# Kernel tuning notes

Measured on AMD Instinct MI355X. Metric: run time of the kernel, lower is better.

Reference implementation:

```python
import jax, jax.numpy as jnp
import numpy as np
import math

# Model dims (see shape_source)
N_EMBD = 2048
QK_H = 128      # per-head qk dim
V_H = 128       # per-head v dim
Q_DIM = N_EMBD                 # 2048 -> 16 query heads
N_HEAD = Q_DIM // QK_H         # 16
KV_HEAD = N_HEAD // 4          # 4 (GQA)
K_DIM = KV_HEAD * QK_H         # 512
V_DIM = KV_HEAD * V_H          # 512
D_KV = K_DIM + V_DIM           # 1024, S6 channel dim
D_STATE = 16                   # S6 state size
DT_RANK = math.ceil(D_KV / 16) # 'auto' -> 64
WINDOW = 512
B, T = 1, 4096


def setup_inputs() -> dict:
    key = jax.random.key(0)
    ks = jax.random.split(key, 8)
    x = jax.random.normal(ks[0], (B, T, N_EMBD), jnp.float32)
    W_attn = jax.random.normal(ks[1], (Q_DIM + K_DIM + V_DIM, N_EMBD), jnp.float32) * 0.02
    # S6 params (canonical Mamba S6 init: A = -exp(A_log), A_log = log(1..N))
    A_log = jnp.log(jnp.arange(1, D_STATE + 1, dtype=jnp.float32))[None, :] * jnp.ones((D_KV, 1), jnp.float32)
    x_proj_w = jax.random.normal(ks[2], (DT_RANK + 2 * D_STATE, D_KV), jnp.float32) * 0.02
    dt_proj_w = jax.random.normal(ks[3], (D_KV, DT_RANK), jnp.float32) * 0.02
    dt_proj_b = jax.random.normal(ks[4], (D_KV,), jnp.float32) * 0.1
    D_param = jnp.ones((D_KV,), jnp.float32)
    W_o = jax.random.normal(ks[5], (N_EMBD, Q_DIM), jnp.float32) * 0.02
    return dict(x=x, W_attn=W_attn, A_log=A_log, x_proj_w=x_proj_w,
                dt_proj_w=dt_proj_w, dt_proj_b=dt_proj_b, D_param=D_param,
                W_o=W_o, window_size=WINDOW)


def s6_scan(u, A_log, x_proj_w, dt_proj_w, dt_proj_b, D_param):
    """Canonical S6 selective scan. u: (B, T, D) -> (B, T, D)."""
    Bb, Tt, D = u.shape
    N = A_log.shape[1]
    dt_rank = dt_proj_w.shape[1]
    x_dbl = jnp.einsum('btd,ed->bte', u, x_proj_w)          # (B,T,dt_rank+2N)
    dt, Bm, Cm = jnp.split(x_dbl, [dt_rank, dt_rank + N], axis=-1)
    delta = jax.nn.softplus(jnp.einsum('btr,dr->btd', dt, dt_proj_w) + dt_proj_b)  # (B,T,D)
    A = -jnp.exp(A_log)                                      # (D,N), negative
    dA = jnp.exp(delta[..., None] * A)                       # (B,T,D,N)
    dBu = delta[..., None] * Bm[:, :, None, :] * u[..., None]  # (B,T,D,N)

    def step(h, inp):
        dA_t, dBu_t, C_t = inp
        h = dA_t * h + dBu_t                                 # (B,D,N)
        y = jnp.einsum('bdn,bn->bd', h, C_t)
        return h, y

    h0 = jnp.zeros((Bb, D, N), u.dtype)
    _, ys = jax.lax.scan(step, h0,
                         (dA.transpose(1, 0, 2, 3), dBu.transpose(1, 0, 2, 3), Cm.transpose(1, 0, 2)))
    y = ys.transpose(1, 0, 2)                                # (B,T,D)
    return y + D_param * u


def sliding_window_attn(q, k, v, window, scale):
    """Causal sliding-window attention; query i attends to j in [i-(window-1), i].
    q: (B,T,H,dh), k/v: (B,T,Hk,dh). Blockwise with one look-back block."""
    Bb, Tt, H, dh = q.shape
    Hk = k.shape[2]
    G = H // Hk
    k = jnp.repeat(k, G, axis=2)
    v = jnp.repeat(v, G, axis=2)
    W = window
    nb = Tt // W
    # (B,H,nb,W,dh)
    qb = q.reshape(Bb, nb, W, H, dh).transpose(0, 3, 1, 2, 4)
    kb = k.reshape(Bb, nb, W, H, dh).transpose(0, 3, 1, 2, 4)
    vb = v.reshape(Bb, nb, W, H, dh).transpose(0, 3, 1, 2, 4)
    # previous block (zeros for first block)
    kprev = jnp.pad(kb, ((0, 0), (0, 0), (1, 0), (0, 0), (0, 0)))[:, :, :nb]
    vprev = jnp.pad(vb, ((0, 0), (0, 0), (1, 0), (0, 0), (0, 0)))[:, :, :nb]
    k2 = jnp.concatenate([kprev, kb], axis=3)                # (B,H,nb,2W,dh)
    v2 = jnp.concatenate([vprev, vb], axis=3)
    scores = jnp.einsum('bhwid,bhwjd->bhwij', qb * scale, k2)  # (B,H,nb,W,2W)
    i = jnp.arange(W)[:, None]
    j = jnp.arange(2 * W)[None, :]
    rel = i + W - j                                          # absolute i - j
    base_mask = (rel >= 0) & (rel <= W - 1)                  # causal & within window
    blk = jnp.arange(nb)[:, None, None]
    valid = base_mask[None] & ((j[None] >= W) | (blk > 0))   # first block: no look-back
    neg = jnp.finfo(jnp.float32).max
    scores = jnp.where(valid[None, None], scores, -neg)
    attn = jax.nn.softmax(scores.astype(jnp.float32), axis=-1).astype(q.dtype)
    out = jnp.einsum('bhwij,bhwjd->bhwid', attn, v2)         # (B,H,nb,W,dh)
    return out.transpose(0, 2, 3, 1, 4).reshape(Bb, Tt, H, dh)


def reference(x, W_attn, A_log, x_proj_w, dt_proj_w, dt_proj_b, D_param, W_o, window_size):
    Bb, Tt, C = x.shape
    qkv = jnp.einsum('btc,oc->bto', x, W_attn)
    q = qkv[..., :Q_DIM]
    kv = qkv[..., Q_DIM:]
    kv = s6_scan(kv, A_log, x_proj_w, dt_proj_w, dt_proj_b, D_param)
    k = kv[..., :K_DIM]
    v = kv[..., K_DIM:]
    q = q.reshape(Bb, Tt, N_HEAD, QK_H)
    k = k.reshape(Bb, Tt, KV_HEAD, QK_H)
    v = v.reshape(Bb, Tt, KV_HEAD, V_H)
    scale = 1.0 / math.sqrt(QK_H)
    y = sliding_window_attn(q, k, v, window_size, scale)     # (B,T,H,v_h)
    y = y.reshape(Bb, Tt, -1)
    return jnp.einsum('bto,no->btn', y, W_o)
```

## Files before the change

### kernel.cpp

```cpp
#include <hip/hip_runtime.h>
#include <hip/hip_bf16.h>

typedef __hip_bfloat16 bf16;
typedef __attribute__((ext_vector_type(8))) short bf16x8;
typedef __attribute__((ext_vector_type(4))) float f32x4;

#define T_SEQ 4096
#define NEMBD 2048
#define QKVD  3072
#define QDIM  2048
#define DKV   1024
#define KDIM  512
#define NH    16
#define DH    128
#define NST   16
#define DTR   64
#define WIN   512
#define NCHUNK 128
#define CLEN   32

__device__ inline float bf2f(bf16 x) { return __bfloat162float(x); }

struct F8 { float v[8]; };

__device__ inline F8 load_b8(const bf16* p) {
  union { uint4 q; unsigned short s[8]; } u;
  u.q = *reinterpret_cast<const uint4*>(p);
  F8 r;
#pragma unroll
  for (int i = 0; i < 8; i++) r.v[i] = __uint_as_float((unsigned)u.s[i] << 16);
  return r;
}

__device__ inline F8 load8(const void* base, size_t idx, int f32flag) {
  if (f32flag) {
    const float4* p = reinterpret_cast<const float4*>((const float*)base + idx);
    float4 a = p[0], b = p[1];
    F8 r;
    r.v[0]=a.x; r.v[1]=a.y; r.v[2]=a.z; r.v[3]=a.w;
    r.v[4]=b.x; r.v[5]=b.y; r.v[6]=b.z; r.v[7]=b.w;
    return r;
  }
  return load_b8((const bf16*)base + idx);
}

__device__ inline float load1(const void* base, size_t idx, int f32flag) {
  return f32flag ? ((const float*)base)[idx] : bf2f(((const bf16*)base)[idx]);
}

__device__ inline unsigned short f2b_bits(float f) {
  bf16 h = __float2bfloat16(f);
  union { bf16 h; unsigned short u; } c; c.h = h; return c.u;
}

__device__ inline ushort4 pack4(float a, float b, float c, float d) {
  ushort4 r; r.x = f2b_bits(a); r.y = f2b_bits(b); r.z = f2b_bits(c); r.w = f2b_bits(d);
  return r;
}

__device__ inline void gld_lds16(const void* g, void* l) {
  __builtin_amdgcn_global_load_lds(
      (const __attribute__((address_space(1))) unsigned int*)g,
      (__attribute__((address_space(3))) unsigned int*)l, 16, 0, 0);
}

__global__ void detect_dtype(const unsigned short* __restrict__ x, int* __restrict__ flag) {
  if (threadIdx.x == 0 && blockIdx.x == 0) {
    int c = 0;
    for (int i = 0; i < 128; i++) {
      float v = __uint_as_float((unsigned)x[i] << 16);
      float a = fabsf(v);
      if (a >= 1e-8f && a <= 1e4f) c++;
    }
    flag[0] = (c >= 120) ? 0 : 1;
  }
}

__global__ __launch_bounds__(256) void cvt_bf16(
    const void* __restrict__ in, const int* __restrict__ dflag,
    unsigned short* __restrict__ out, int n8)
{
  int i = blockIdx.x * 256 + threadIdx.x;
  if (i >= n8) return;
  const int f = dflag[0];
  F8 v = load8(in, (size_t)i * 8, f);
  ushort4* o = (ushort4*)(out + (size_t)i * 8);
  o[0] = pack4(v.v[0], v.v[1], v.v[2], v.v[3]);
  o[1] = pack4(v.v[4], v.v[5], v.v[6], v.v[7]);
}

__global__ __launch_bounds__(512, 2) void gemm_wide(
    const unsigned short* __restrict__ A, const unsigned short* __restrict__ B,
    int M, int N, int K, int mode,
    bf16* __restrict__ oq, bf16* __restrict__ ou, float* __restrict__ oc)
{
  __shared__ unsigned short lds[2][384 * 64];
  const int tid = threadIdx.x;
  const int wave = tid >> 6, lane = tid & 63;
  const int quad = lane >> 4, l16 = lane & 15;
  const int wm = wave >> 1, wn = wave & 1;
  const int nbx = N >> 7;
  const int nwg = gridDim.x;
  const int chunk = nwg >> 3;
  const int swz = (blockIdx.x & 7) * chunk + (blockIdx.x >> 3);
  const int bm = (swz / nbx) * 256, bn = (swz % nbx) * 128;

  const int lrow = lane >> 3;
  const int lslot = (lane & 7) ^ lrow;
  const unsigned short* Abase = A + (size_t)(bm + wave * 8 + lrow) * K + lslot * 8;
  const unsigned short* Bbase = B + (size_t)(bn + wave * 8 + lrow) * K + lslot * 8;

  const int x7 = l16 & 7;
  const int s0 = ((0 + quad) ^ x7) * 8;
  const int s1 = ((4 + quad) ^ x7) * 8;
  const int arow0 = (wm * 64 + l16) * 64;
  const int brow0 = (256 + wn * 64 + l16) * 64;

  f32x4 acc[4][4];
#pragma unroll
  for (int i = 0; i < 4; i++)
#pragma unroll
    for (int j = 0; j < 4; j++) acc[i][j] = f32x4{0.f, 0.f, 0.f, 0.f};

  const int NT = K >> 6;

#pragma unroll
  for (int grp = 0; grp < 4; grp++)
    gld_lds16(Abase + (size_t)grp * 64 * K, &lds[0][(grp * 64 + wave * 8) * 64]);
#pragma unroll
  for (int grp = 0; grp < 2; grp++)
    gld_lds16(Bbase + (size_t)grp * 64 * K, &lds[0][(256 + grp * 64 + wave * 8) * 64]);
#pragma unroll
  for (int grp = 0; grp < 4; grp++)
    gld_lds16(Abase + (size_t)grp * 64 * K + 64, &lds[1][(grp * 64 + wave * 8) * 64]);
#pragma unroll
  for (int grp = 0; grp < 2; grp++)
    gld_lds16(Bbase + (size_t)grp * 64 * K + 64, &lds[1][(256 + grp * 64 + wave * 8) * 64]);
  asm volatile("s_waitcnt vmcnt(6)" ::: "memory");
  __builtin_amdgcn_sched_barrier(0);
  __builtin_amdgcn_s_barrier();

#define MM(m, n) \
  acc[m][n] = __builtin_amdgcn_mfma_f32_16x16x32_bf16(aF[m][0], bF[n][0], acc[m][n], 0, 0, 0); \
  acc[m][n] = __builtin_amdgcn_mfma_f32_16x16x32_bf16(aF[m][1], bF[n][1], acc[m][n], 0, 0, 0);

  for (int g = 0; g < NT; ++g) {
    const unsigned short* L = lds[g & 1];
    unsigned short* Lw = (unsigned short*)L;
    const bool stF = (g + 2) < NT;
    const size_t kF = (size_t)(g + 2) * 64;

    bf16x8 aF[4][2], bF[4][2];

#pragma unroll
    for (int m = 0; m < 4; m++) {
      aF[m][0] = *(const bf16x8*)&L[arow0 + m * 1024 + s0];
      aF[m][1] = *(const bf16x8*)&L[arow0 + m * 1024 + s1];
    }
    bF[0][0] = *(const bf16x8*)&L[brow0 +    0 + s0];
    bF[0][1] = *(const bf16x8*)&L[brow0 +    0 + s1];
    bF[1][0] = *(const bf16x8*)&L[brow0 + 1024 + s0];
    bF[1][1] = *(const bf16x8*)&L[brow0 + 1024 + s1];
    __builtin_amdgcn_s_barrier();
    if (stF) {
#pragma unroll
      for (int grp = 0; grp < 4; grp++)
        gld_lds16(Abase + (size_t)grp * 64 * K + kF, &Lw[(grp * 64 + wave * 8) * 64]);
    }
    __builtin_amdgcn_s_setprio(1);
    MM(0,0); MM(0,1); MM(1,0); MM(1,1);
    MM(2,0); MM(2,1); MM(3,0); MM(3,1);
    __builtin_amdgcn_s_setprio(0);
    __builtin_amdgcn_s_barrier();

    bF[2][0] = *(const bf16x8*)&L[brow0 + 2048 + s0];
    bF[2][1] = *(const bf16x8*)&L[brow0 + 2048 + s1];
    bF[3][0] = *(const bf16x8*)&L[brow0 + 3072 + s0];
    bF[3][1] = *(const bf16x8*)&L[brow0 + 3072 + s1];
    __builtin_amdgcn_s_barrier();
    if (stF) {
#pragma unroll
      for (int grp = 0; grp < 2; grp++)
        gld_lds16(Bbase + (size_t)grp * 64 * K + kF, &Lw[(256 + grp * 64 + wave * 8) * 64]);
    }
    __builtin_amdgcn_s_setprio(1);
    MM(0,2); MM(0,3); MM(1,2); MM(1,3);
    MM(2,2); MM(2,3); MM(3,2); MM(3,3);
    __builtin_amdgcn_s_setprio(0);
    if (stF) { asm volatile("s_waitcnt vmcnt(6)" ::: "memory"); }
    else     { asm volatile("s_waitcnt vmcnt(0)" ::: "memory"); }
    __builtin_amdgcn_sched_barrier(0);
    __builtin_amdgcn_s_barrier();
  }
#undef MM

#pragma unroll
  for (int m = 0; m < 4; m++)
#pragma unroll
    for (int n = 0; n < 4; n++) {
      int gm0 = bm + wm * 64 + m * 16 + quad * 4;
      int gn  = bn + wn * 64 + n * 16 + l16;
#pragma unroll
      for (int r = 0; r < 4; r++) {
        int gm = gm0 + r;
        float v = acc[m][n][r];
        if (mode == 0) {
          if (gn < QDIM) oq[(size_t)gm * QDIM + gn] = __float2bfloat16(v);
          else           ou[(size_t)gm * DKV + (gn - QDIM)] = __float2bfloat16(v);
        } else {
          oc[(size_t)gm * N + gn] = v;
        }
      }
    }
}

__global__ __launch_bounds__(256) void xdbl_mfma(
    const bf16* __restrict__ u, const unsigned short* __restrict__ xpw_bf,
    float* __restrict__ xd)
{
  __shared__ unsigned short Us[64 * 32];
  __shared__ unsigned short Ws[96 * 32];
  const int tid = threadIdx.x;
  const int wave = tid >> 6, lane = tid & 63;
  const int quad = lane >> 4, l16 = lane & 15;
  const int t0 = blockIdx.x * 64;
  const unsigned short* ub = (const unsigned short*)u;

  f32x4 acc[6];
#pragma unroll
  for (int j = 0; j < 6; j++) acc[j] = f32x4{0.f, 0.f, 0.f, 0.f};

  const int urow = tid >> 2, ucol = (tid & 3) * 8;
  const int wrow0 = tid >> 2, wcol0 = (tid & 3) * 8;
  const int wrow1 = (256 + tid) >> 2;

  uint4 upre = *(const uint4*)(ub + (size_t)(t0 + urow) * DKV + ucol);
  uint4 wpre0 = *(const uint4*)(xpw_bf + (size_t)wrow0 * DKV + wcol0);
  uint4 wpre1 = (tid < 128) ? *(const uint4*)(xpw_bf + (size_t)wrow1 * DKV + wcol0)
                            : uint4{0, 0, 0, 0};

  for (int k0 = 0; k0 < DKV; k0 += 32) {
    __syncthreads();
    *(uint4*)&Us[urow * 32 + ucol] = upre;
    *(uint4*)&Ws[wrow0 * 32 + wcol0] = wpre0;
    if (tid < 128) *(uint4*)&Ws[wrow1 * 32 + wcol0] = wpre1;
    __syncthreads();

    int kn = (k0 + 32 < DKV) ? (k0 + 32) : k0;
    upre  = *(const uint4*)(ub + (size_t)(t0 + urow) * DKV + kn + ucol);
    wpre0 = *(const uint4*)(xpw_bf + (size_t)wrow0 * DKV + kn + wcol0);
    if (tid < 128) wpre1 = *(const uint4*)(xpw_bf + (size_t)wrow1 * DKV + kn + wcol0);

    bf16x8 a = *(const bf16x8*)&Us[(wave * 16 + l16) * 32 + quad * 8];
#pragma unroll
    for (int j = 0; j < 6; j++) {
      bf16x8 b = *(const bf16x8*)&Ws[(j * 16 + l16) * 32 + quad * 8];
      acc[j] = __builtin_amdgcn_mfma_f32_16x16x32_bf16(a, b, acc[j], 0, 0, 0);
    }
  }

#pragma unroll
  for (int j = 0; j < 6; j++)
#pragma unroll
    for (int r = 0; r < 4; r++) {
      int t = t0 + wave * 16 + quad * 4 + r;
      xd[(size_t)t * 96 + j * 16 + l16] = acc[j][r];
    }
}

__global__ __launch_bounds__(256) void delta_mfma(
    const float* __restrict__ xd, const unsigned short* __restrict__ dtw_bf,
    const void* __restrict__ dtb, const int* __restrict__ dflag,
    bf16* __restrict__ delta)
{
  __shared__ unsigned short Xs[64 * 72];
  __shared__ unsigned short Ws[128 * 72];
  const int tid = threadIdx.x;
  const int wave = tid >> 6, lane = tid & 63;
  const int quad = lane >> 4, l16 = lane & 15;
  const int t0 = blockIdx.y * 64, d0 = blockIdx.x * 128;

  for (int e = tid; e < 64 * 8; e += 256) {
    int row = e >> 3, c8 = (e & 7) * 8;
    const float* p = xd + (size_t)(t0 + row) * 96 + c8;
    float4 a = *(const float4*)p, b = *(const float4*)(p + 4);
    *(ushort4*)&Xs[row * 72 + c8]     = pack4(a.x, a.y, a.z, a.w);
    *(ushort4*)&Xs[row * 72 + c8 + 4] = pack4(b.x, b.y, b.z, b.w);
  }
  for (int e = tid; e < 128 * 8; e += 256) {
    int row = e >> 3, c8 = (e & 7) * 8;
    *(uint4*)&Ws[row * 72 + c8] = *(const uint4*)(dtw_bf + (size_t)(d0 + row) * DTR + c8);
  }
  __syncthreads();

  bf16x8 a0 = *(const bf16x8*)&Xs[(wave * 16 + l16) * 72 + quad * 8];
  bf16x8 a1 = *(const bf16x8*)&Xs[(wave * 16 + l16) * 72 + 32 + quad * 8];

  f32x4 acc[8];
#pragma unroll
  for (int j = 0; j < 8; j++) {
    bf16x8 b0 = *(const bf16x8*)&Ws[(j * 16 + l16) * 72 + quad * 8];
    bf16x8 b1 = *(const bf16x8*)&Ws[(j * 16 + l16) * 72 + 32 + quad * 8];
    acc[j] = __builtin_amdgcn_mfma_f32_16x16x32_bf16(a0, b0, f32x4{0.f, 0.f, 0.f, 0.f}, 0, 0, 0);
    acc[j] = __builtin_amdgcn_mfma_f32_16x16x32_bf16(a1, b1, acc[j], 0, 0, 0);
  }

  const int f = dflag[0];
#pragma unroll
  for (int j = 0; j < 8; j++) {
    int d = d0 + j * 16 + l16;
    float bias = load1(dtb, d, f);
#pragma unroll
    for (int r = 0; r < 4; r++) {
      int t = t0 + wave * 16 + quad * 4 + r;
      float v = acc[j][r] + bias;
      float sp = fmaxf(v, 0.f) + log1pf(expf(-fabsf(v)));
      delta[(size_t)t * DKV + d] = __float2bfloat16(sp);
    }
  }
}

__global__ __launch_bounds__(256) void scan_pass1(
    const bf16* __restrict__ delta, const bf16* __restrict__ u,
    const float* __restrict__ xd, const void* __restrict__ A_log,
    const int* __restrict__ dflag, float* __restrict__ Pb, float* __restrict__ Hl)
{
  const int gid = blockIdx.x * 256 + threadIdx.x;
  const int c = gid >> 14;
  const int r = gid & 16383;
  const int d = r >> 4, n = r & 15;
  const int f = dflag[0];
  const float A = -expf(load1(A_log, d * NST + n, f));
  float p = 1.f, h = 0.f;
  const int t0 = c * CLEN;
  for (int tt = 0; tt < CLEN; tt++) {
    int t = t0 + tt;
    float dl = bf2f(delta[(size_t)t * DKV + d]);
    float uu = bf2f(u[(size_t)t * DKV + d]);
    float bm = xd[(size_t)t * 96 + DTR + n];
    float a = expf(dl * A);
    h = a * h + dl * bm * uu;
    p *= a;
  }
  Pb[gid] = p;
  Hl[gid] = h;
}

__global__ __launch_bounds__(256) void scan_combine(
    float* __restrict__ Pb, const float* __restrict__ Hl)
{
  const int idx = blockIdx.x * 256 + threadIdx.x;
  float run = 0.f;
  for (int c = 0; c < NCHUNK; c++) {
    size_t off = (size_t)c * 16384 + idx;
    float p = Pb[off], hl = Hl[off];
    Pb[off] = run;
    run = p * run + hl;
  }
}

__global__ __launch_bounds__(256) void scan_pass2(
    const bf16* __restrict__ delta, bf16* __restrict__ u,
    const float* __restrict__ xd, const void* __restrict__ A_log,
    const void* __restrict__ Dp, const int* __restrict__ dflag,
    const float* __restrict__ Hin)
{
  const int gid = blockIdx.x * 256 + threadIdx.x;
  const int c = gid >> 14;
  const int r = gid & 16383;
  const int d = r >> 4, n = r & 15;
  const int f = dflag[0];
  const float A = -expf(load1(A_log, d * NST + n, f));
  const float dpar = load1(Dp, d, f);
  float h = Hin[gid];
  const int t0 = c * CLEN;
  for (int tt = 0; tt < CLEN; tt++) {
    int t = t0 + tt;
    float dl = bf2f(delta[(size_t)t * DKV + d]);
    float uu = bf2f(u[(size_t)t * DKV + d]);
    float bm = xd[(size_t)t * 96 + DTR + n];
    float cm = xd[(size_t)t * 96 + DTR + NST + n];
    float a = expf(dl * A);
    h = a * h + dl * bm * uu;
    float part = h * cm;
    part += __shfl_xor(part, 1);
    part += __shfl_xor(part, 2);
    part += __shfl_xor(part, 4);
    part += __shfl_xor(part, 8);
    if (n == 0) u[(size_t)t * DKV + d] = __float2bfloat16(part + dpar * uu);
  }
}

__global__ __launch_bounds__(256) void vtrans(
    const bf16* __restrict__ kv, unsigned short* __restrict__ vt)
{
  __shared__ float tile[64][68];
  const int tt0 = blockIdx.x * 64, d0 = blockIdx.y * 64;
  const int tid = threadIdx.x;
  for (int e = tid; e < 64 * 8; e += 256) {
    int row = e >> 3, c8 = (e & 7) * 8;
    F8 v = load_b8(kv + (size_t)(tt0 + row) * DKV + KDIM + d0 + c8);
#pragma unroll
    for (int j = 0; j < 8; j++) tile[row][c8 + j] = v.v[j];
  }
  __syncthreads();
  for (int e = tid; e < 64 * 8; e += 256) {
    int dd = e >> 3, t8 = (e & 7) * 8;
    float vv[8];
#pragma unroll
    for (int j = 0; j < 8; j++) vv[j] = tile[t8 + j][dd];
    ushort4* o = (ushort4*)(vt + (size_t)(d0 + dd) * T_SEQ + tt0 + t8);
    o[0] = pack4(vv[0], vv[1], vv[2], vv[3]);
    o[1] = pack4(vv[4], vv[5], vv[6], vv[7]);
  }
}

__global__ __launch_bounds__(256, 4) void attn_mfma(
    const bf16* __restrict__ q, const bf16* __restrict__ kv,
    const unsigned short* __restrict__ vt, bf16* __restrict__ y)
{
  __shared__ unsigned short Ks[32 * 136];
  __shared__ unsigned short Vts[128 * 40];
  __shared__ unsigned short Ps[4][16 * 40];
  const int tid = threadIdx.x;
  const int wave = tid >> 6, lane = tid & 63;
  const int quad = lane >> 4, l16 = lane & 15;
  const int qt = blockIdx.x, h = blockIdx.y, kvh = h >> 2;
  const int t0 = qt * 64;
  const float scale = 0.088388347648318447f;

  bf16x8 af[4];
#pragma unroll
  for (int s = 0; s < 4; s++)
    af[s] = *(const bf16x8*)(q + (size_t)(t0 + wave * 16 + l16) * QDIM
                             + h * DH + s * 32 + quad * 8);

  const int krow = tid >> 4, kc8 = (tid & 15) * 8;
  const int vrow = tid >> 2, vc8 = (tid & 3) * 8;
  const bf16* kgp = kv + (size_t)kvh * DH;
  const unsigned short* vgp = vt + (size_t)(kvh * DH) * T_SEQ;

  float m_r[4], l_p[4];
  f32x4 O[8];
#pragma unroll
  for (int r = 0; r < 4; r++) { m_r[r] = -1e30f; l_p[r] = 0.f; }
#pragma unroll
  for (int dt = 0; dt < 8; dt++) O[dt] = f32x4{0.f, 0.f, 0.f, 0.f};

  const int kb_start = (t0 > WIN - 1) ? ((t0 - (WIN - 1)) >> 5) : 0;
  const int kb_end = (t0 + 63) >> 5;

  uint4 kp0, kp1, vp0, vp1;
  {
    const int kb = kb_start;
    kp0 = *(const uint4*)(kgp + (size_t)(kb * 32 + krow) * DKV + kc8);
    kp1 = *(const uint4*)(kgp + (size_t)(kb * 32 + 16 + krow) * DKV + kc8);
    vp0 = *(const uint4*)(vgp + (size_t)vrow * T_SEQ + kb * 32 + vc8);
    vp1 = *(const uint4*)(vgp + (size_t)(vrow + 64) * T_SEQ + kb * 32 + vc8);
  }

  for (int kb = kb_start; kb <= kb_end; kb++) {
    __syncthreads();
    *(uint4*)&Ks[krow * 136 + kc8]        = kp0;
    *(uint4*)&Ks[(krow + 16) * 136 + kc8] = kp1;
    *(uint4*)&Vts[vrow * 40 + vc8]        = vp0;
    *(uint4*)&Vts[(vrow + 64) * 40 + vc8] = vp1;
    __syncthreads();

    if (kb < kb_end) {
      const int kn = kb + 1;
      kp0 = *(const uint4*)(kgp + (size_t)(kn * 32 + krow) * DKV + kc8);
      kp1 = *(const uint4*)(kgp + (size_t)(kn * 32 + 16 + krow) * DKV + kc8);
      vp0 = *(const uint4*)(vgp + (size_t)vrow * T_SEQ + kn * 32 + vc8);
      vp1 = *(const uint4*)(vgp + (size_t)(vrow + 64) * T_SEQ + kn * 32 + vc8);
    }

    f32x4 S0 = f32x4{0.f, 0.f, 0.f, 0.f}, S1 = f32x4{0.f, 0.f, 0.f, 0.f};
#pragma unroll
    for (int s = 0; s < 4; s++) {
      bf16x8 b0 = *(const bf16x8*)&Ks[(l16) * 136 + s * 32 + quad * 8];
      bf16x8 b1 = *(const bf16x8*)&Ks[(16 + l16) * 136 + s * 32 + quad * 8];
      S0 = __builtin_amdgcn_mfma_f32_16x16x32_bf16(af[s], b0, S0, 0, 0, 0);
      S1 = __builtin_amdgcn_mfma_f32_16x16x32_bf16(af[s], b1, S1, 0, 0, 0);
    }

    const int ka0 = kb * 32 + l16;
    const int ka1 = ka0 + 16;
    const bool full = (kb * 32 >= t0 + 63 - (WIN - 1)) && (kb * 32 + 31 <= t0);

    float v0r[4], v1r[4];
    bool x0r[4], x1r[4];
    bool ok = true;
#pragma unroll
    for (int r = 0; r < 4; r++) {
      int qa = t0 + wave * 16 + quad * 4 + r;
      float v0 = S0[r] * scale, v1 = S1[r] * scale;
      bool x0 = true, x1 = true;
      if (!full) {
        x0 = (ka0 <= qa) && (ka0 > qa - WIN);
        x1 = (ka1 <= qa) && (ka1 > qa - WIN);
        if (!x0) v0 = -1e30f;
        if (!x1) v1 = -1e30f;
      }
      v0r[r] = v0; v1r[r] = v1; x0r[r] = x0; x1r[r] = x1;
      ok = ok && (fmaxf(v0, v1) <= m_r[r] + 8.f);
    }

    if (!__all((int)ok)) {
#pragma unroll
      for (int r = 0; r < 4; r++) {
        float rm = fmaxf(v0r[r], v1r[r]);
        rm = fmaxf(rm, __shfl_xor(rm, 1));
        rm = fmaxf(rm, __shfl_xor(rm, 2));
        rm = fmaxf(rm, __shfl_xor(rm, 4));
        rm = fmaxf(rm, __shfl_xor(rm, 8));
        float mnew = fmaxf(m_r[r], rm);
        float al = __expf(m_r[r] - mnew);
        m_r[r] = mnew;
        l_p[r] *= al;
#pragma unroll
        for (int dt = 0; dt < 8; dt++) O[dt][r] *= al;
      }
    }

#pragma unroll
    for (int r = 0; r < 4; r++) {
      float p0 = x0r[r] ? __expf(v0r[r] - m_r[r]) : 0.f;
      float p1 = x1r[r] ? __expf(v1r[r] - m_r[r]) : 0.f;
      l_p[r] += p0 + p1;
      Ps[wave][(quad * 4 + r) * 40 + l16]      = f2b_bits(p0);
      Ps[wave][(quad * 4 + r) * 40 + 16 + l16] = f2b_bits(p1);
    }

    bf16x8 pa = *(const bf16x8*)&Ps[wave][l16 * 40 + quad * 8];
#pragma unroll
    for (int dt = 0; dt < 8; dt++) {
      bf16x8 b = *(const bf16x8*)&Vts[(dt * 16 + l16) * 40 + quad * 8];
      O[dt] = __builtin_amdgcn_mfma_f32_16x16x32_bf16(pa, b, O[dt], 0, 0, 0);
    }
  }

  float inv[4];
#pragma unroll
  for (int r = 0; r < 4; r++) {
    float l = l_p[r];
    l += __shfl_xor(l, 1);
    l += __shfl_xor(l, 2);
    l += __shfl_xor(l, 4);
    l += __shfl_xor(l, 8);
    inv[r] = 1.f / l;
  }
#pragma unroll
  for (int dt = 0; dt < 8; dt++)
#pragma unroll
    for (int r = 0; r < 4; r++) {
      int row = t0 + wave * 16 + quad * 4 + r;
      y[(size_t)row * QDIM + h * DH + dt * 16 + l16] = __float2bfloat16(O[dt][r] * inv[r]);
    }
}

extern "C" void kernel_launch(void* const* d_in, const int* in_sizes, int n_in,
                              void* d_out, int out_size, void* d_ws, size_t ws_size,
                              hipStream_t stream)
{
  const void* x      = d_in[0];
  const void* W_attn = d_in[1];
  const void* A_log  = d_in[2];
  const void* xpw    = d_in[3];
  const void* dtw    = d_in[4];
  const void* dtb    = d_in[5];
  const void* Dp     = d_in[6];
  const void* W_o    = d_in[7];

  char* ws = (char*)d_ws;
  int*   dflag = (int*)ws;   ws += 256;
  bf16*  u     = (bf16*)ws;  ws += (size_t)T_SEQ * DKV * 2;
  float* xd    = (float*)ws; ws += (size_t)T_SEQ * 96 * 4;
  char*  yreg  = ws;
  bf16*  delta = (bf16*)ws;  ws += (size_t)T_SEQ * DKV * 2;
  ws += (size_t)64 * DKV * NST * 4;
  ws += (size_t)64 * DKV * NST * 4;
  unsigned short* x_bf  = (unsigned short*)ws; ws += (size_t)T_SEQ * NEMBD * 2;
  unsigned short* wa_bf = (unsigned short*)ws; ws += (size_t)QKVD * NEMBD * 2;
  unsigned short* wo_bf = (unsigned short*)ws; ws += (size_t)NEMBD * QDIM * 2;
  unsigned short* vt    = (unsigned short*)ws; ws += (size_t)KDIM * T_SEQ * 2;
  unsigned short* xpw_bf = (unsigned short*)ws; ws += (size_t)96 * DKV * 2;
  unsigned short* dtw_bf = (unsigned short*)ws; ws += (size_t)DKV * DTR * 2;
  bf16*  y     = (bf16*)yreg;

  float* Pb = (float*)x_bf;
  float* Hl = Pb + (size_t)NCHUNK * DKV * NST;

  bf16*  q_bf = (bf16*)d_out;
  float* out  = (float*)d_out;

  detect_dtype<<<1, 64, 0, stream>>>((const unsigned short*)x, dflag);
  cvt_bf16<<<(T_SEQ * NEMBD / 8 + 255) / 256, 256, 0, stream>>>(x, dflag, x_bf, T_SEQ * NEMBD / 8);
  cvt_bf16<<<(QKVD * NEMBD / 8 + 255) / 256, 256, 0, stream>>>(W_attn, dflag, wa_bf, QKVD * NEMBD / 8);
  cvt_bf16<<<(NEMBD * QDIM / 8 + 255) / 256, 256, 0, stream>>>(W_o, dflag, wo_bf, NEMBD * QDIM / 8);
  cvt_bf16<<<(96 * DKV / 8 + 255) / 256, 256, 0, stream>>>(xpw, dflag, xpw_bf, 96 * DKV / 8);
  cvt_bf16<<<(DKV * DTR / 8 + 255) / 256, 256, 0, stream>>>(dtw, dflag, dtw_bf, DKV * DTR / 8);

  gemm_wide<<<(T_SEQ / 256) * (QKVD / 128), 512, 0, stream>>>(
      x_bf, wa_bf, T_SEQ, QKVD, NEMBD, 0, q_bf, u, nullptr);
  xdbl_mfma<<<T_SEQ / 64, 256, 0, stream>>>(u, xpw_bf, xd);
  delta_mfma<<<dim3(DKV / 128, T_SEQ / 64), 256, 0, stream>>>(xd, dtw_bf, dtb, dflag, delta);
  scan_pass1<<<NCHUNK * 64, 256, 0, stream>>>(delta, u, xd, A_log, dflag, Pb, Hl);
  scan_combine<<<64, 256, 0, stream>>>(Pb, Hl);
  scan_pass2<<<NCHUNK * 64, 256, 0, stream>>>(delta, u, xd, A_log, Dp, dflag, Pb);
  vtrans<<<dim3(T_SEQ / 64, KDIM / 64), 256, 0, stream>>>(u, vt);
  attn_mfma<<<dim3(T_SEQ / 64, NH), 256, 0, stream>>>(q_bf, u, vt, y);
  gemm_wide<<<(T_SEQ / 256) * (QDIM / 128), 512, 0, stream>>>(
      (const unsigned short*)y, wo_bf, T_SEQ, QDIM, QDIM, 1, nullptr, nullptr, out);
}
```

Measured before the change: 445.6 us.

## Widen attention key blocks to 64, fuse conversion launches, retune scan chunking

The attention kernel now processes 64-key blocks instead of 32, with larger LDS tiles and s_setprio hints around the MFMA sections. This halves loop iterations, syncs and softmax bookkeeping per block, at the cost of more LDS and lower occupancy (launch bounds 4→3). The five bf16 conversion kernels are merged into one launch to cut launch overhead. The scan chunk configuration changes from 128×32 to 64×64, which halves scan parallelism but shortens the combine step.

```diff
diff --git a/kernel.cpp b/kernel.cpp
--- a/kernel.cpp
+++ b/kernel.cpp
@@ -16,8 +16,8 @@
 #define NST   16
 #define DTR   64
 #define WIN   512
-#define NCHUNK 128
-#define CLEN   32
+#define NCHUNK 64
+#define CLEN   64
 
 __device__ inline float bf2f(bf16 x) { return __bfloat162float(x); }
 
@@ -76,15 +76,32 @@
   }
 }
 
-__global__ __launch_bounds__(256) void cvt_bf16(
-    const void* __restrict__ in, const int* __restrict__ dflag,
-    unsigned short* __restrict__ out, int n8)
+#define N8_X   (T_SEQ * NEMBD / 8)
+#define N8_WA  (QKVD * NEMBD / 8)
+#define N8_WO  (NEMBD * QDIM / 8)
+#define N8_XPW (96 * DKV / 8)
+#define N8_DTW (DKV * DTR / 8)
+#define N8_TOT (N8_X + N8_WA + N8_WO + N8_XPW + N8_DTW)
+
+__global__ __launch_bounds__(256) void cvt_all(
+    const void* __restrict__ x, const void* __restrict__ wa,
+    const void* __restrict__ wo, const void* __restrict__ xpw,
+    const void* __restrict__ dtw, const int* __restrict__ dflag,
+    unsigned short* __restrict__ xo, unsigned short* __restrict__ wao,
+    unsigned short* __restrict__ woo, unsigned short* __restrict__ xpwo,
+    unsigned short* __restrict__ dtwo)
 {
   int i = blockIdx.x * 256 + threadIdx.x;
-  if (i >= n8) return;
+  if (i >= N8_TOT) return;
   const int f = dflag[0];
-  F8 v = load8(in, (size_t)i * 8, f);
-  ushort4* o = (ushort4*)(out + (size_t)i * 8);
+  const void* in; unsigned short* out; size_t idx;
+  if      (i < N8_X)                        { in = x;   out = xo;   idx = i; }
+  else if (i < N8_X + N8_WA)                { in = wa;  out = wao;  idx = i - N8_X; }
+  else if (i < N8_X + N8_WA + N8_WO)        { in = wo;  out = woo;  idx = i - (N8_X + N8_WA); }
+  else if (i < N8_X + N8_WA + N8_WO + N8_XPW) { in = xpw; out = xpwo; idx = i - (N8_X + N8_WA + N8_WO); }
+  else                                      { in = dtw; out = dtwo; idx = i - (N8_X + N8_WA + N8_WO + N8_XPW); }
+  F8 v = load8(in, idx * 8, f);
+  ushort4* o = (ushort4*)(out + idx * 8);
   o[0] = pack4(v.v[0], v.v[1], v.v[2], v.v[3]);
   o[1] = pack4(v.v[4], v.v[5], v.v[6], v.v[7]);
 }
@@ -415,13 +432,13 @@
   }
 }
 
-__global__ __launch_bounds__(256, 4) void attn_mfma(
+__global__ __launch_bounds__(256, 3) void attn_mfma(
     const bf16* __restrict__ q, const bf16* __restrict__ kv,
     const unsigned short* __restrict__ vt, bf16* __restrict__ y)
 {
-  __shared__ unsigned short Ks[32 * 136];
-  __shared__ unsigned short Vts[128 * 40];
-  __shared__ unsigned short Ps[4][16 * 40];
+  __shared__ unsigned short Ks[64 * 136];
+  __shared__ unsigned short Vts[128 * 72];
+  __shared__ unsigned short Ps[4][16 * 72];
   const int tid = threadIdx.x;
   const int wave = tid >> 6, lane = tid & 63;
   const int quad = lane >> 4, l16 = lane & 15;
@@ -436,7 +453,7 @@
                              + h * DH + s * 32 + quad * 8);
 
   const int krow = tid >> 4, kc8 = (tid & 15) * 8;
-  const int vrow = tid >> 2, vc8 = (tid & 3) * 8;
+  const int vrow = tid >> 2, vc = (tid & 3) * 8;
   const bf16* kgp = kv + (size_t)kvh * DH;
   const unsigned short* vgp = vt + (size_t)(kvh * DH) * T_SEQ;
 
@@ -447,69 +464,90 @@
 #pragma unroll
   for (int dt = 0; dt < 8; dt++) O[dt] = f32x4{0.f, 0.f, 0.f, 0.f};
 
-  const int kb_start = (t0 > WIN - 1) ? ((t0 - (WIN - 1)) >> 5) : 0;
-  const int kb_end = (t0 + 63) >> 5;
-
-  uint4 kp0, kp1, vp0, vp1;
+  const int kb_start = (t0 > WIN - 1) ? ((t0 - (WIN - 1)) >> 6) : 0;
+  const int kb_end = t0 >> 6;
+
+  uint4 kp[4], vp[4];
   {
     const int kb = kb_start;
-    kp0 = *(const uint4*)(kgp + (size_t)(kb * 32 + krow) * DKV + kc8);
-    kp1 = *(const uint4*)(kgp + (size_t)(kb * 32 + 16 + krow) * DKV + kc8);
-    vp0 = *(const uint4*)(vgp + (size_t)vrow * T_SEQ + kb * 32 + vc8);
-    vp1 = *(const uint4*)(vgp + (size_t)(vrow + 64) * T_SEQ + kb * 32 + vc8);
+#pragma unroll
+    for (int j = 0; j < 4; j++)
+      kp[j] = *(const uint4*)(kgp + (size_t)(kb * 64 + krow + j * 16) * DKV + kc8);
+#pragma unroll
+    for (int rr = 0; rr < 2; rr++)
+#pragma unroll
+      for (int jj = 0; jj < 2; jj++)
+        vp[rr * 2 + jj] = *(const uint4*)(vgp + (size_t)(vrow + rr * 64) * T_SEQ
+                                          + kb * 64 + vc + jj * 32);
   }
 
   for (int kb = kb_start; kb <= kb_end; kb++) {
     __syncthreads();
-    *(uint4*)&Ks[krow * 136 + kc8]        = kp0;
-    *(uint4*)&Ks[(krow + 16) * 136 + kc8] = kp1;
-    *(uint4*)&Vts[vrow * 40 + vc8]        = vp0;
-    *(uint4*)&Vts[(vrow + 64) * 40 + vc8] = vp1;
+#pragma unroll
+    for (int j = 0; j < 4; j++)
+      *(uint4*)&Ks[(krow + j * 16) * 136 + kc8] = kp[j];
+#pragma unroll
+    for (int rr = 0; rr < 2; rr++)
+#pragma unroll
+      for (int jj = 0; jj < 2; jj++)
+        *(uint4*)&Vts[(vrow + rr * 64) * 72 + vc + jj * 32] = vp[rr * 2 + jj];
     __syncthreads();
 
     if (kb < kb_end) {
       const int kn = kb + 1;
-      kp0 = *(const uint4*)(kgp + (size_t)(kn * 32 + krow) * DKV + kc8);
-      kp1 = *(const uint4*)(kgp + (size_t)(kn * 32 + 16 + krow) * DKV + kc8);
-      vp0 = *(const uint4*)(vgp + (size_t)vrow * T_SEQ + kn * 32 + vc8);
-      vp1 = *(const uint4*)(vgp + (size_t)(vrow + 64) * T_SEQ + kn * 32 + vc8);
-    }
-
-    f32x4 S0 = f32x4{0.f, 0.f, 0.f, 0.f}, S1 = f32x4{0.f, 0.f, 0.f, 0.f};
+#pragma unroll
+      for (int j = 0; j < 4; j++)
+        kp[j] = *(const uint4*)(kgp + (size_t)(kn * 64 + krow + j * 16) * DKV + kc8);
+#pragma unroll
+      for (int rr = 0; rr < 2; rr++)
+#pragma unroll
+        for (int jj = 0; jj < 2; jj++)
+          vp[rr * 2 + jj] = *(const uint4*)(vgp + (size_t)(vrow + rr * 64) * T_SEQ
+                                            + kn * 64 + vc + jj * 32);
+    }
+
+    f32x4 S[4];
+#pragma unroll
+    for (int j = 0; j < 4; j++) S[j] = f32x4{0.f, 0.f, 0.f, 0.f};
+    __builtin_amdgcn_s_setprio(1);
 #pragma unroll
     for (int s = 0; s < 4; s++) {
-      bf16x8 b0 = *(const bf16x8*)&Ks[(l16) * 136 + s * 32 + quad * 8];
-      bf16x8 b1 = *(const bf16x8*)&Ks[(16 + l16) * 136 + s * 32 + quad * 8];
-      S0 = __builtin_amdgcn_mfma_f32_16x16x32_bf16(af[s], b0, S0, 0, 0, 0);
-      S1 = __builtin_amdgcn_mfma_f32_16x16x32_bf16(af[s], b1, S1, 0, 0, 0);
-    }
-
-    const int ka0 = kb * 32 + l16;
-    const int ka1 = ka0 + 16;
-    const bool full = (kb * 32 >= t0 + 63 - (WIN - 1)) && (kb * 32 + 31 <= t0);
-
-    float v0r[4], v1r[4];
-    bool x0r[4], x1r[4];
+#pragma unroll
+      for (int j = 0; j < 4; j++) {
+        bf16x8 b = *(const bf16x8*)&Ks[(j * 16 + l16) * 136 + s * 32 + quad * 8];
+        S[j] = __builtin_amdgcn_mfma_f32_16x16x32_bf16(af[s], b, S[j], 0, 0, 0);
+      }
+    }
+    __builtin_amdgcn_s_setprio(0);
+
+    const bool full = (kb * 64 >= t0 + 63 - (WIN - 1)) && (kb * 64 + 63 <= t0);
+
+    float v_r[4][4];
+    bool x_r[4][4];
     bool ok = true;
 #pragma unroll
     for (int r = 0; r < 4; r++) {
       int qa = t0 + wave * 16 + quad * 4 + r;
-      float v0 = S0[r] * scale, v1 = S1[r] * scale;
-      bool x0 = true, x1 = true;
-      if (!full) {
-        x0 = (ka0 <= qa) && (ka0 > qa - WIN);
-        x1 = (ka1 <= qa) && (ka1 > qa - WIN);
-        if (!x0) v0 = -1e30f;
-        if (!x1) v1 = -1e30f;
+      float rm4 = -1e30f;
+#pragma unroll
+      for (int j = 0; j < 4; j++) {
+        int ka = kb * 64 + j * 16 + l16;
+        float vv = S[j][r] * scale;
+        bool xx = true;
+        if (!full) {
+          xx = (ka <= qa) && (ka > qa - WIN);
+          if (!xx) vv = -1e30f;
+        }
+        v_r[r][j] = vv; x_r[r][j] = xx;
+        rm4 = fmaxf(rm4, vv);
       }
-      v0r[r] = v0; v1r[r] = v1; x0r[r] = x0; x1r[r] = x1;
-      ok = ok && (fmaxf(v0, v1) <= m_r[r] + 8.f);
+      ok = ok && (rm4 <= m_r[r] + 8.f);
     }
 
     if (!__all((int)ok)) {
 #pragma unroll
       for (int r = 0; r < 4; r++) {
-        float rm = fmaxf(v0r[r], v1r[r]);
+        float rm = fmaxf(fmaxf(v_r[r][0], v_r[r][1]), fmaxf(v_r[r][2], v_r[r][3]));
         rm = fmaxf(rm, __shfl_xor(rm, 1));
         rm = fmaxf(rm, __shfl_xor(rm, 2));
         rm = fmaxf(rm, __shfl_xor(rm, 4));
@@ -525,19 +563,29 @@
 
 #pragma unroll
     for (int r = 0; r < 4; r++) {
-      float p0 = x0r[r] ? __expf(v0r[r] - m_r[r]) : 0.f;
-      float p1 = x1r[r] ? __expf(v1r[r] - m_r[r]) : 0.f;
-      l_p[r] += p0 + p1;
-      Ps[wave][(quad * 4 + r) * 40 + l16]      = f2b_bits(p0);
-      Ps[wave][(quad * 4 + r) * 40 + 16 + l16] = f2b_bits(p1);
-    }
-
-    bf16x8 pa = *(const bf16x8*)&Ps[wave][l16 * 40 + quad * 8];
+      float p0 = x_r[r][0] ? __expf(v_r[r][0] - m_r[r]) : 0.f;
+      float p1 = x_r[r][1] ? __expf(v_r[r][1] - m_r[r]) : 0.f;
+      float p2 = x_r[r][2] ? __expf(v_r[r][2] - m_r[r]) : 0.f;
+      float p3 = x_r[r][3] ? __expf(v_r[r][3] - m_r[r]) : 0.f;
+      l_p[r] += (p0 + p1) + (p2 + p3);
+      int prow = (quad * 4 + r) * 72;
+      Ps[wave][prow + l16]      = f2b_bits(p0);
+      Ps[wave][prow + 16 + l16] = f2b_bits(p1);
+      Ps[wave][prow + 32 + l16] = f2b_bits(p2);
+      Ps[wave][prow + 48 + l16] = f2b_bits(p3);
+    }
+
+    bf16x8 pa0 = *(const bf16x8*)&Ps[wave][l16 * 72 + quad * 8];
+    bf16x8 pa1 = *(const bf16x8*)&Ps[wave][l16 * 72 + 32 + quad * 8];
+    __builtin_amdgcn_s_setprio(1);
 #pragma unroll
     for (int dt = 0; dt < 8; dt++) {
-      bf16x8 b = *(const bf16x8*)&Vts[(dt * 16 + l16) * 40 + quad * 8];
-      O[dt] = __builtin_amdgcn_mfma_f32_16x16x32_bf16(pa, b, O[dt], 0, 0, 0);
-    }
+      bf16x8 b0 = *(const bf16x8*)&Vts[(dt * 16 + l16) * 72 + quad * 8];
+      bf16x8 b1 = *(const bf16x8*)&Vts[(dt * 16 + l16) * 72 + 32 + quad * 8];
+      O[dt] = __builtin_amdgcn_mfma_f32_16x16x32_bf16(pa0, b0, O[dt], 0, 0, 0);
+      O[dt] = __builtin_amdgcn_mfma_f32_16x16x32_bf16(pa1, b1, O[dt], 0, 0, 0);
+    }
+    __builtin_amdgcn_s_setprio(0);
   }
 
   float inv[4];
@@ -595,11 +643,8 @@
   float* out  = (float*)d_out;
 
   detect_dtype<<<1, 64, 0, stream>>>((const unsigned short*)x, dflag);
-  cvt_bf16<<<(T_SEQ * NEMBD / 8 + 255) / 256, 256, 0, stream>>>(x, dflag, x_bf, T_SEQ * NEMBD / 8);
-  cvt_bf16<<<(QKVD * NEMBD / 8 + 255) / 256, 256, 0, stream>>>(W_attn, dflag, wa_bf, QKVD * NEMBD / 8);
-  cvt_bf16<<<(NEMBD * QDIM / 8 + 255) / 256, 256, 0, stream>>>(W_o, dflag, wo_bf, NEMBD * QDIM / 8);
-  cvt_bf16<<<(96 * DKV / 8 + 255) / 256, 256, 0, stream>>>(xpw, dflag, xpw_bf, 96 * DKV / 8);
-  cvt_bf16<<<(DKV * DTR / 8 + 255) / 256, 256, 0, stream>>>(dtw, dflag, dtw_bf, DKV * DTR / 8);
+  cvt_all<<<(N8_TOT + 255) / 256, 256, 0, stream>>>(
+      x, W_attn, W_o, xpw, dtw, dflag, x_bf, wa_bf, wo_bf, xpw_bf, dtw_bf);
 
   gemm_wide<<<(T_SEQ / 256) * (QKVD / 128), 512, 0, stream>>>(
       x_bf, wa_bf, T_SEQ, QKVD, NEMBD, 0, q_bf, u, nullptr);
```

Measured after the change: 490.2 us. 10.0% more time.
